# Optimization experiments

Hardware: AMD Instinct MI355X
Metric: run time of the kernel (lower is better)

## Reference

```python
import jax, jax.numpy as jnp
import numpy as np

DIM = 1024
HEADS = 16
DIM_HEAD = 64
INNER = HEADS * DIM_HEAD  # 1024
SCALE = DIM_HEAD ** -0.5


def setup_inputs() -> dict:
    key = jax.random.key(0)
    k1, k2, k3, k4 = jax.random.split(key, 4)
    x = jax.random.normal(k1, (4, 2048, DIM), dtype=jnp.float32)
    # nn.Linear weight is [out, in]; store transposed [in, out] for x @ W
    w_qkv = jax.random.normal(k2, (DIM, 3 * INNER), dtype=jnp.float32) * (DIM ** -0.5)
    w_out = jax.random.normal(k3, (INNER, DIM), dtype=jnp.float32) * (INNER ** -0.5)
    b_out = jax.random.normal(k4, (DIM,), dtype=jnp.float32) * 0.01
    return {"x": x, "w_qkv": w_qkv, "w_out": w_out, "b_out": b_out}


def reference(x, w_qkv, w_out, b_out):
    b, n, _ = x.shape
    qkv = x @ w_qkv                                   # [b, n, 3*inner]
    q, k, v = jnp.split(qkv, 3, axis=-1)
    # 'b n (h d) -> b h n d'
    def split_heads(t):
        return t.reshape(b, n, HEADS, DIM_HEAD).transpose(0, 2, 1, 3)
    q, k, v = split_heads(q), split_heads(k), split_heads(v)
    attn = jnp.einsum('bhnd,bhmd->bhnm', q, k) * SCALE  # [b, h, n, n]
    attn = jax.nn.softmax(attn, axis=-1)
    out = jnp.einsum('bhnm,bhmd->bhnd', attn, v)        # [b, h, n, d]
    out = out.transpose(0, 2, 1, 3).reshape(b, n, INNER)  # 'b h n d -> b n (h d)'
    return out @ w_out + b_out
```

## Files before the change

kernel.cpp:

```cpp
#include <hip/hip_runtime.h>
#include <hip/hip_bf16.h>
#include <cmath>

typedef float f4 __attribute__((ext_vector_type(4)));
typedef float f32x4 __attribute__((ext_vector_type(4)));
typedef short bf16x8 __attribute__((ext_vector_type(8)));
typedef unsigned short us4 __attribute__((ext_vector_type(4)));
typedef unsigned short us;
typedef unsigned short us4a __attribute__((ext_vector_type(4))) __attribute__((may_alias));
typedef short bf16x8a __attribute__((ext_vector_type(8))) __attribute__((may_alias));

#define TOK   2048
#define NBAT  4
#define NH    16
#define DH    64
#define MODEL 1024
#define MTOT  (NBAT*TOK)
#define NQKV  (3*MODEL)
#define QSCALE_LOG2E 0.1803368801111204f
#define CBIAS 16.0f
#define BUF_ELEMS ((size_t)MTOT*MODEL)

__device__ inline us f2bf(float x) {
    union { __hip_bfloat16 h; us u; } cv;
    cv.h = __float2bfloat16(x);
    return cv.u;
}

__device__ inline us f2bf_fast(float x) {
    unsigned int u = __float_as_uint(x);
    u += 0x7FFF + ((u >> 16) & 1);
    return (us)(u >> 16);
}

__global__ __launch_bounds__(256)
void cvt_k(const float* __restrict__ X, us* __restrict__ Y)
{
    const size_t i = ((size_t)blockIdx.x * 256 + threadIdx.x) << 2;
    f4 v = *(const f4*)&X[i];
    us4 u;
    #pragma unroll
    for (int j = 0; j < 4; ++j) u[j] = f2bf(v[j]);
    *(us4*)&Y[i] = u;
}

__global__ __launch_bounds__(256)
void tcvt_k(const float* __restrict__ W, us* __restrict__ WT, int K, int N)
{
    __shared__ float T[64][65];
    const int n0 = blockIdx.x << 6, k0 = blockIdx.y << 6;
    const int tid = threadIdx.x;
    const int r = tid >> 4, c4 = (tid & 15) << 2;
    #pragma unroll
    for (int i = 0; i < 4; ++i) {
        const int kr = r + (i << 4);
        *(f4*)&T[kr][c4] = *(const f4*)&W[(size_t)(k0 + kr) * N + n0 + c4];
    }
    __syncthreads();
    #pragma unroll
    for (int i = 0; i < 4; ++i) {
        const int nr = r + (i << 4);
        us4 u;
        #pragma unroll
        for (int j = 0; j < 4; ++j) u[j] = f2bf(T[c4 + j][nr]);
        *(us4*)&WT[(size_t)(n0 + nr) * K + k0 + c4] = u;
    }
}

#define GEMM_BODY(Aptr, Bptr, KDIM)                                            \
    __shared__ us As[128][72];                                                 \
    __shared__ us Bs[128][72];                                                 \
    const int tid = threadIdx.x;                                               \
    const int lane = tid & 63;                                                 \
    const int w = tid >> 6, wr = w >> 1, wc = w & 1;                           \
    const int l15 = lane & 15, lg = lane >> 4;                                 \
    const int bm = blockIdx.x << 7, bn = blockIdx.y << 7;                      \
    int srow[4], soff[4];                                                      \
    _Pragma("unroll")                                                          \
    for (int i = 0; i < 4; ++i) {                                              \
        const int c = tid + (i << 8);                                          \
        srow[i] = c >> 3; soff[i] = (c & 7) << 3;                              \
    }                                                                          \
    const us* Ag = Aptr + (size_t)bm * (KDIM);                                 \
    const us* Bg = Bptr + (size_t)bn * (KDIM);                                 \
    bf16x8 ra[4], rb[4];                                                       \
    _Pragma("unroll")                                                          \
    for (int i = 0; i < 4; ++i) {                                              \
        ra[i] = *(const bf16x8*)&Ag[(size_t)srow[i] * (KDIM) + soff[i]];       \
        rb[i] = *(const bf16x8*)&Bg[(size_t)srow[i] * (KDIM) + soff[i]];       \
    }                                                                          \
    f32x4 acc[4][4];                                                           \
    _Pragma("unroll")                                                          \
    for (int m = 0; m < 4; ++m)                                                \
        _Pragma("unroll")                                                      \
        for (int n = 0; n < 4; ++n) acc[m][n] = (f32x4){0.f, 0.f, 0.f, 0.f};   \
    const int NS = (KDIM) / 64;                                                \
    for (int s = 0; s < NS; ++s) {                                             \
        _Pragma("unroll")                                                      \
        for (int i = 0; i < 4; ++i) {                                          \
            *(bf16x8*)&As[srow[i]][soff[i]] = ra[i];                           \
            *(bf16x8*)&Bs[srow[i]][soff[i]] = rb[i];                           \
        }                                                                      \
        __syncthreads();                                                       \
        if (s + 1 < NS) {                                                      \
            const int k0 = (s + 1) << 6;                                       \
            _Pragma("unroll")                                                  \
            for (int i = 0; i < 4; ++i) {                                      \
                ra[i] = *(const bf16x8*)&Ag[(size_t)srow[i] * (KDIM) + k0 + soff[i]]; \
                rb[i] = *(const bf16x8*)&Bg[(size_t)srow[i] * (KDIM) + k0 + soff[i]]; \
            }                                                                  \
        }                                                                      \
        _Pragma("unroll")                                                      \
        for (int kk = 0; kk < 2; ++kk) {                                       \
            bf16x8 af[4], bfr[4];                                              \
            _Pragma("unroll")                                                  \
            for (int m = 0; m < 4; ++m)                                        \
                af[m] = *(const bf16x8*)&As[(wr << 6) + (m << 4) + l15][(kk << 5) + (lg << 3)]; \
            _Pragma("unroll")                                                  \
            for (int n = 0; n < 4; ++n)                                        \
                bfr[n] = *(const bf16x8*)&Bs[(wc << 6) + (n << 4) + l15][(kk << 5) + (lg << 3)]; \
            _Pragma("unroll")                                                  \
            for (int m = 0; m < 4; ++m)                                        \
                _Pragma("unroll")                                              \
                for (int n = 0; n < 4; ++n)                                    \
                    acc[m][n] = __builtin_amdgcn_mfma_f32_16x16x32_bf16(af[m], bfr[n], acc[m][n], 0, 0, 0); \
        }                                                                      \
        __syncthreads();                                                       \
    }

__global__ __launch_bounds__(256)
void qkv_mfma_k(const us* __restrict__ Abf, const us* __restrict__ BT,
                us* __restrict__ qb, us* __restrict__ kb, us* __restrict__ vt)
{
    GEMM_BODY(Abf, BT, MODEL)

    const int cb  = bn + (wc << 6);
    const int sel = cb >> 10;
    const int cc0 = cb & 1023;
    const int bb  = bm >> 11;
    const int nnb = (bm & (TOK - 1)) + (wr << 6);

    if (sel < 2) {
        us* p = sel ? kb : qb;
        const float mul = sel ? 1.f : QSCALE_LOG2E;
        #pragma unroll
        for (int n = 0; n < 4; ++n) {
            const int cc = cc0 + (n << 4) + l15;
            const int h = cc >> 6, dd = cc & 63;
            us* pp = p + ((size_t)(bb * NH + h) * TOK) * DH + dd;
            #pragma unroll
            for (int m = 0; m < 4; ++m)
                #pragma unroll
                for (int r = 0; r < 4; ++r) {
                    const int nn = nnb + (m << 4) + (lg << 2) + r;
                    pp[(size_t)nn * DH] = f2bf(acc[m][n][r] * mul);
                }
        }
    } else {
        #pragma unroll
        for (int n = 0; n < 4; ++n) {
            const int cc = cc0 + (n << 4) + l15;
            const int h = cc >> 6, dd = cc & 63;
            #pragma unroll
            for (int m = 0; m < 4; ++m) {
                const int nn = nnb + (m << 4) + (lg << 2);
                us4 u;
                #pragma unroll
                for (int r = 0; r < 4; ++r) u[r] = f2bf(acc[m][n][r]);
                *(us4*)&vt[((size_t)(bb * NH + h) * DH + dd) * TOK + nn] = u;
            }
        }
    }
}

__global__ __launch_bounds__(256)
void out_mfma_k(const us* __restrict__ Abf, const us* __restrict__ BT,
                const float* __restrict__ bias, float* __restrict__ C)
{
    GEMM_BODY(Abf, BT, MODEL)

    #pragma unroll
    for (int n = 0; n < 4; ++n) {
        const int c = bn + (wc << 6) + (n << 4) + l15;
        const float bv = bias[c];
        #pragma unroll
        for (int m = 0; m < 4; ++m) {
            const int row = bm + (wr << 6) + (m << 4) + (lg << 2);
            #pragma unroll
            for (int r = 0; r < 4; ++r)
                C[(size_t)(row + r) * MODEL + c] = acc[m][n][r] + bv;
        }
    }
}

__global__ __launch_bounds__(256)
void attn7_k(const us* __restrict__ qb, const us* __restrict__ kb,
             const us* __restrict__ vt, us* __restrict__ ob)
{
    __shared__ __align__(16) us Ks[2][64 * 64];
    __shared__ __align__(16) us Vs[2][64 * 64];
    __shared__ __align__(16) us Ps[4][16][64];

    const int tid  = threadIdx.x;
    const int lane = tid & 63;
    const int w    = tid >> 6;
    const int l15  = lane & 15;
    const int lg   = lane >> 4;
    const int bh   = blockIdx.y;
    const int qw   = (blockIdx.x << 7) + (w << 5);

    const us* Q = qb + (size_t)bh * TOK * DH;
    const us* K = kb + (size_t)bh * TOK * DH;
    const us* V = vt + (size_t)bh * DH * TOK;

    int sr[2], sc[2], sl[2];
    #pragma unroll
    for (int i = 0; i < 2; ++i) {
        const int idx = tid + (i << 8);
        sr[i] = idx >> 3;
        sc[i] = idx & 7;
        sl[i] = sr[i] * 64 + ((sc[i] ^ (sr[i] & 7)) << 3);
    }

    const int cs0 = (((0 << 2) + lg) ^ (l15 & 7)) << 3;
    const int cs1 = (((1 << 2) + lg) ^ (l15 & 7)) << 3;

    us4a* pw[4];
    #pragma unroll
    for (int j = 0; j < 4; ++j) {
        const int chunk = ((j << 1) + (lg >> 1)) ^ (l15 & 7);
        pw[j] = (us4a*)&Ps[w][l15][(chunk << 3) + ((lg & 1) << 2)];
    }
    const bf16x8a* pr0 = (const bf16x8a*)&Ps[w][l15][(lg ^ (l15 & 7)) << 3];
    const bf16x8a* pr1 = (const bf16x8a*)&Ps[w][l15][((4 + lg) ^ (l15 & 7)) << 3];

    bf16x8 onesf;
    #pragma unroll
    for (int i = 0; i < 8; ++i) onesf[i] = (short)0x3F80;

    bf16x8 qf[2][2];
    #pragma unroll
    for (int qs = 0; qs < 2; ++qs)
        #pragma unroll
        for (int h = 0; h < 2; ++h)
            qf[qs][h] = *(const bf16x8*)&Q[(size_t)(qw + (qs << 4) + l15) * DH + (h << 5) + (lg << 3)];

    f32x4 lacc[2];
    f32x4 o[2][4];
    #pragma unroll
    for (int qs = 0; qs < 2; ++qs) {
        lacc[qs] = (f32x4){0.f, 0.f, 0.f, 0.f};
        #pragma unroll
        for (int dj = 0; dj < 4; ++dj) o[qs][dj] = (f32x4){0.f, 0.f, 0.f, 0.f};
    }

    const int NT = TOK / 64;
    bf16x8 krg[2], vrg[2];

    #pragma unroll
    for (int i = 0; i < 2; ++i) {
        krg[i] = *(const bf16x8*)&K[(size_t)sr[i] * DH + (sc[i] << 3)];
        vrg[i] = *(const bf16x8*)&V[(size_t)sr[i] * TOK + (sc[i] << 3)];
    }
    #pragma unroll
    for (int i = 0; i < 2; ++i) {
        *(bf16x8*)&Ks[0][sl[i]] = krg[i];
        *(bf16x8*)&Vs[0][sl[i]] = vrg[i];
    }

    int cur = 0;
    for (int t = 0; t < NT; ++t) {
        if (t + 1 < NT) {
            const int k0 = (t + 1) << 6;
            #pragma unroll
            for (int i = 0; i < 2; ++i) {
                krg[i] = *(const bf16x8*)&K[(size_t)(k0 + sr[i]) * DH + (sc[i] << 3)];
                vrg[i] = *(const bf16x8*)&V[(size_t)sr[i] * TOK + k0 + (sc[i] << 3)];
            }
        }
        __syncthreads();

        bf16x8 vf[4][2], kf[4][2];
        #pragma unroll
        for (int dj = 0; dj < 4; ++dj) {
            vf[dj][0] = *(const bf16x8*)&Vs[cur][((dj << 4) + l15) * 64 + cs0];
            vf[dj][1] = *(const bf16x8*)&Vs[cur][((dj << 4) + l15) * 64 + cs1];
        }
        #pragma unroll
        for (int j = 0; j < 4; ++j) {
            kf[j][0] = *(const bf16x8*)&Ks[cur][((j << 4) + l15) * 64 + cs0];
            kf[j][1] = *(const bf16x8*)&Ks[cur][((j << 4) + l15) * 64 + cs1];
        }

        #pragma unroll
        for (int qs = 0; qs < 2; ++qs) {
            f32x4 st[4];
            __builtin_amdgcn_s_setprio(1);
            #pragma unroll
            for (int j = 0; j < 4; ++j) {
                f32x4 a = (f32x4){-CBIAS, -CBIAS, -CBIAS, -CBIAS};
                a = __builtin_amdgcn_mfma_f32_16x16x32_bf16(kf[j][0], qf[qs][0], a, 0, 0, 0);
                a = __builtin_amdgcn_mfma_f32_16x16x32_bf16(kf[j][1], qf[qs][1], a, 0, 0, 0);
                st[j] = a;
            }
            __builtin_amdgcn_s_setprio(0);

            #pragma unroll
            for (int j = 0; j < 4; ++j) {
                us4a u;
                u[0] = f2bf_fast(__builtin_amdgcn_exp2f(st[j][0]));
                u[1] = f2bf_fast(__builtin_amdgcn_exp2f(st[j][1]));
                u[2] = f2bf_fast(__builtin_amdgcn_exp2f(st[j][2]));
                u[3] = f2bf_fast(__builtin_amdgcn_exp2f(st[j][3]));
                *pw[j] = u;
            }
            const bf16x8 pf0 = *pr0;
            const bf16x8 pf1 = *pr1;

            __builtin_amdgcn_s_setprio(1);
            #pragma unroll
            for (int dj = 0; dj < 4; ++dj) {
                o[qs][dj] = __builtin_amdgcn_mfma_f32_16x16x32_bf16(vf[dj][0], pf0, o[qs][dj], 0, 0, 0);
                o[qs][dj] = __builtin_amdgcn_mfma_f32_16x16x32_bf16(vf[dj][1], pf1, o[qs][dj], 0, 0, 0);
            }
            lacc[qs] = __builtin_amdgcn_mfma_f32_16x16x32_bf16(onesf, pf0, lacc[qs], 0, 0, 0);
            lacc[qs] = __builtin_amdgcn_mfma_f32_16x16x32_bf16(onesf, pf1, lacc[qs], 0, 0, 0);
            __builtin_amdgcn_s_setprio(0);
        }

        if (t + 1 < NT) {
            #pragma unroll
            for (int i = 0; i < 2; ++i) {
                *(bf16x8*)&Ks[cur ^ 1][sl[i]] = krg[i];
                *(bf16x8*)&Vs[cur ^ 1][sl[i]] = vrg[i];
            }
        }
        cur ^= 1;
    }

    const int b = bh >> 4;
    const int hh = bh & 15;
    #pragma unroll
    for (int qs = 0; qs < 2; ++qs) {
        const int q = qw + (qs << 4) + l15;
        const float inv = 1.f / lacc[qs][0];
        #pragma unroll
        for (int dj = 0; dj < 4; ++dj) {
            us4 u;
            #pragma unroll
            for (int r = 0; r < 4; ++r) u[r] = f2bf(o[qs][dj][r] * inv);
            *(us4*)&ob[(size_t)(b * TOK + q) * MODEL + (hh << 6) + (dj << 4) + (lg << 2)] = u;
        }
    }
}

extern "C" void kernel_launch(void* const* d_in, const int* in_sizes, int n_in,
                              void* d_out, int out_size, void* d_ws, size_t ws_size,
                              hipStream_t stream)
{
    const float* x     = (const float*)d_in[0];
    const float* w_qkv = (const float*)d_in[1];
    const float* w_out = (const float*)d_in[2];
    const float* b_out = (const float*)d_in[3];
    float* out = (float*)d_out;

    us* qb   = (us*)d_ws;
    us* kb   = qb + BUF_ELEMS;
    us* vt   = kb + BUF_ELEMS;
    us* xbf  = vt + BUF_ELEMS;
    us* wqT  = xbf + BUF_ELEMS;
    us* woT  = wqT + (size_t)NQKV * MODEL;
    us* atto = woT + (size_t)MODEL * MODEL;

    dim3 blk(256);
    cvt_k<<<(MTOT * MODEL) / 1024, blk, 0, stream>>>(x, xbf);
    tcvt_k<<<dim3(NQKV / 64, MODEL / 64), blk, 0, stream>>>(w_qkv, wqT, MODEL, NQKV);
    tcvt_k<<<dim3(MODEL / 64, MODEL / 64), blk, 0, stream>>>(w_out, woT, MODEL, MODEL);
    qkv_mfma_k<<<dim3(MTOT / 128, NQKV / 128), blk, 0, stream>>>(xbf, wqT, qb, kb, vt);
    attn7_k<<<dim3(TOK / 128, NBAT * NH), blk, 0, stream>>>(qb, kb, vt, atto);
    out_mfma_k<<<dim3(MTOT / 128, MODEL / 128), blk, 0, stream>>>(atto, woT, b_out, out);
}
```

Measured before the change: 212.1 us.

## Double attention block to 512 threads so each K/V tile serves 256 queries

The attention kernel now runs 8 waves per block covering 256 query rows instead of 4 waves covering 128. Each 64-key K/V tile staged in shared memory is therefore reused by twice as many queries, and each thread loads one 16-byte chunk per tile instead of two. The barrier moves to the top of the loop, before the next tile's global loads are issued. The price is half as many blocks (512 total), larger barriers across 8 waves, and a different per-CU occupancy balance.

```diff
diff --git a/kernel.cpp b/kernel.cpp
--- a/kernel.cpp
+++ b/kernel.cpp
@@ -193,13 +193,13 @@
     }
 }
 
-__global__ __launch_bounds__(256)
-void attn7_k(const us* __restrict__ qb, const us* __restrict__ kb,
+__global__ __launch_bounds__(512)
+void attn8_k(const us* __restrict__ qb, const us* __restrict__ kb,
              const us* __restrict__ vt, us* __restrict__ ob)
 {
     __shared__ __align__(16) us Ks[2][64 * 64];
     __shared__ __align__(16) us Vs[2][64 * 64];
-    __shared__ __align__(16) us Ps[4][16][64];
+    __shared__ __align__(16) us Ps[8][16][64];
 
     const int tid  = threadIdx.x;
     const int lane = tid & 63;
@@ -207,20 +207,15 @@
     const int l15  = lane & 15;
     const int lg   = lane >> 4;
     const int bh   = blockIdx.y;
-    const int qw   = (blockIdx.x << 7) + (w << 5);
+    const int qw   = (blockIdx.x << 8) + (w << 5);
 
     const us* Q = qb + (size_t)bh * TOK * DH;
     const us* K = kb + (size_t)bh * TOK * DH;
     const us* V = vt + (size_t)bh * DH * TOK;
 
-    int sr[2], sc[2], sl[2];
-    #pragma unroll
-    for (int i = 0; i < 2; ++i) {
-        const int idx = tid + (i << 8);
-        sr[i] = idx >> 3;
-        sc[i] = idx & 7;
-        sl[i] = sr[i] * 64 + ((sc[i] ^ (sr[i] & 7)) << 3);
-    }
+    const int sr = tid >> 3;
+    const int sc = tid & 7;
+    const int sl = sr * 64 + ((sc ^ (sr & 7)) << 3);
 
     const int cs0 = (((0 << 2) + lg) ^ (l15 & 7)) << 3;
     const int cs1 = (((1 << 2) + lg) ^ (l15 & 7)) << 3;
@@ -255,30 +250,22 @@
     }
 
     const int NT = TOK / 64;
-    bf16x8 krg[2], vrg[2];
-
-    #pragma unroll
-    for (int i = 0; i < 2; ++i) {
-        krg[i] = *(const bf16x8*)&K[(size_t)sr[i] * DH + (sc[i] << 3)];
-        vrg[i] = *(const bf16x8*)&V[(size_t)sr[i] * TOK + (sc[i] << 3)];
-    }
-    #pragma unroll
-    for (int i = 0; i < 2; ++i) {
-        *(bf16x8*)&Ks[0][sl[i]] = krg[i];
-        *(bf16x8*)&Vs[0][sl[i]] = vrg[i];
-    }
+    bf16x8 krg, vrg;
+
+    krg = *(const bf16x8*)&K[(size_t)sr * DH + (sc << 3)];
+    vrg = *(const bf16x8*)&V[(size_t)sr * TOK + (sc << 3)];
+    *(bf16x8*)&Ks[0][sl] = krg;
+    *(bf16x8*)&Vs[0][sl] = vrg;
 
     int cur = 0;
     for (int t = 0; t < NT; ++t) {
+        __syncthreads();
+
         if (t + 1 < NT) {
             const int k0 = (t + 1) << 6;
-            #pragma unroll
-            for (int i = 0; i < 2; ++i) {
-                krg[i] = *(const bf16x8*)&K[(size_t)(k0 + sr[i]) * DH + (sc[i] << 3)];
-                vrg[i] = *(const bf16x8*)&V[(size_t)sr[i] * TOK + k0 + (sc[i] << 3)];
-            }
-        }
-        __syncthreads();
+            krg = *(const bf16x8*)&K[(size_t)(k0 + sr) * DH + (sc << 3)];
+            vrg = *(const bf16x8*)&V[(size_t)sr * TOK + k0 + (sc << 3)];
+        }
 
         bf16x8 vf[4][2], kf[4][2];
         #pragma unroll
@@ -329,11 +316,8 @@
         }
 
         if (t + 1 < NT) {
-            #pragma unroll
-            for (int i = 0; i < 2; ++i) {
-                *(bf16x8*)&Ks[cur ^ 1][sl[i]] = krg[i];
-                *(bf16x8*)&Vs[cur ^ 1][sl[i]] = vrg[i];
-            }
+            *(bf16x8*)&Ks[cur ^ 1][sl] = krg;
+            *(bf16x8*)&Vs[cur ^ 1][sl] = vrg;
         }
         cur ^= 1;
     }
@@ -377,6 +361,6 @@
     tcvt_k<<<dim3(NQKV / 64, MODEL / 64), blk, 0, stream>>>(w_qkv, wqT, MODEL, NQKV);
     tcvt_k<<<dim3(MODEL / 64, MODEL / 64), blk, 0, stream>>>(w_out, woT, MODEL, MODEL);
     qkv_mfma_k<<<dim3(MTOT / 128, NQKV / 128), blk, 0, stream>>>(xbf, wqT, qb, kb, vt);
-    attn7_k<<<dim3(TOK / 128, NBAT * NH), blk, 0, stream>>>(qb, kb, vt, atto);
+    attn8_k<<<dim3(TOK / 256, NBAT * NH), dim3(512), 0, stream>>>(qb, kb, vt, atto);
     out_mfma_k<<<dim3(MTOT / 128, MODEL / 128), blk, 0, stream>>>(atto, woT, b_out, out);
 }
```

After: 197.3 us. 7.0% less time.
